# Kernel optimization log

Hardware: AMD Instinct MI355X
Metric: run time of the kernel (lower is better)

Reference implementation:

```python
import jax, jax.numpy as jnp
import numpy as np

EMBED = 1024

def setup_inputs() -> dict:
    key = jax.random.key(0)
    kx, kq, kk, kv = jax.random.split(key, 4)
    x = jax.random.normal(kx, (4, 2048, EMBED), dtype=jnp.float32)
    s = 1.0 / np.sqrt(EMBED)
    Wq = jax.random.normal(kq, (EMBED, EMBED), dtype=jnp.float32) * s
    Wk = jax.random.normal(kk, (EMBED, EMBED), dtype=jnp.float32) * s
    Wv = jax.random.normal(kv, (EMBED, EMBED), dtype=jnp.float32) * s
    return {"x": x, "Wq": Wq, "Wk": Wk, "Wv": Wv}

def reference(x, Wq, Wk, Wv):
    # x: [b, s, e]; nn.Linear(y) = y @ W.T, weights stored [out, in]
    Q = jnp.einsum('bse,oe->bso', x, Wq)
    K = jnp.einsum('bse,oe->bso', x, Wk)
    V = jnp.einsum('bse,oe->bso', x, Wv)
    scale = 1.0 / jnp.sqrt(jnp.asarray(x.shape[-1], x.dtype))
    energy = jnp.einsum('bqe,bke->bqk', Q, K) * scale  # [b, s, s]
    attention = jax.nn.softmax(energy, axis=-1)
    out = jnp.einsum('bqk,bke->bqe', attention, V)
    return out
```

## Files before the change

### kernel.cpp

```cpp
#include <hip/hip_runtime.h>
#include <stdint.h>


typedef __attribute__((ext_vector_type(8))) short bf16x8;
typedef __attribute__((ext_vector_type(4))) float f32x4;

__device__ __forceinline__ float bf2f(uint16_t u) {
    return __uint_as_float(((uint32_t)u) << 16);
}
__device__ __forceinline__ uint16_t f2bf(float f) {
    uint32_t u = __float_as_uint(f);
    uint32_t r = u + 0x7FFFu + ((u >> 16) & 1u);
    return (uint16_t)(r >> 16);
}

__device__ __forceinline__ void gll16(const void* g, void* l) {
    __builtin_amdgcn_global_load_lds(
        (const __attribute__((address_space(1))) uint32_t*)g,
        (__attribute__((address_space(3))) uint32_t*)l,
        16, 0, 0);
}

__global__ __launch_bounds__(256) void cast_f32_bf16(const float* __restrict__ in,
                                                     uint16_t* __restrict__ out,
                                                     int n4) {
    int i = blockIdx.x * 256 + threadIdx.x;
    if (i < n4) {
        float4 v = ((const float4*)in)[i];
        ushort4 o;
        o.x = f2bf(v.x); o.y = f2bf(v.y); o.z = f2bf(v.z); o.w = f2bf(v.w);
        ((ushort4*)out)[i] = o;
    }
}

__global__ __launch_bounds__(256) void transpose_bf16(const uint16_t* __restrict__ in,
                                                      uint16_t* __restrict__ out,
                                                      int rows, int cols) {
    __shared__ uint16_t tile[32][33];
    size_t bo = (size_t)blockIdx.z * rows * cols;
    in += bo; out += bo;
    int bx = blockIdx.x * 32;
    int by = blockIdx.y * 32;
    int tx = threadIdx.x, ty = threadIdx.y;
    #pragma unroll
    for (int i = ty; i < 32; i += 8)
        tile[i][tx] = in[(size_t)(by + i) * cols + bx + tx];
    __syncthreads();
    #pragma unroll
    for (int i = ty; i < 32; i += 8)
        out[(size_t)(bx + i) * rows + by + tx] = tile[tx][i];
}

__global__ __launch_bounds__(256) void softmax_rows(uint16_t* __restrict__ P) {
    const int n = 2048;
    uint16_t* row = P + (size_t)blockIdx.x * n;
    int tid = threadIdx.x;
    int w = tid >> 6, ln = tid & 63;
    float v[8];
    float m = -3.4e38f;
    #pragma unroll
    for (int i = 0; i < 8; i++) { v[i] = bf2f(row[tid + 256 * i]); m = fmaxf(m, v[i]); }
    #pragma unroll
    for (int o = 32; o >= 1; o >>= 1) m = fmaxf(m, __shfl_down(m, o, 64));
    __shared__ float smax[4], ssum[4];
    if (ln == 0) smax[w] = m;
    __syncthreads();
    m = fmaxf(fmaxf(smax[0], smax[1]), fmaxf(smax[2], smax[3]));
    float s = 0.f;
    #pragma unroll
    for (int i = 0; i < 8; i++) { v[i] = __expf(v[i] - m); s += v[i]; }
    #pragma unroll
    for (int o = 32; o >= 1; o >>= 1) s += __shfl_down(s, o, 64);
    if (ln == 0) ssum[w] = s;
    __syncthreads();
    s = ssum[0] + ssum[1] + ssum[2] + ssum[3];
    float inv = 1.f / s;
    #pragma unroll
    for (int i = 0; i < 8; i++) row[tid + 256 * i] = f2bf(v[i] * inv);
}

#define BM 128
#define BN 128
#define BK 32

template <typename OutT>
__global__ __launch_bounds__(256) void gemm_nt(const uint16_t* __restrict__ A,
                                               const uint16_t* __restrict__ B,
                                               OutT* __restrict__ C,
                                               int M, int N, int K, float alpha,
                                               long sA, long sB, long sC) {
    int bz = blockIdx.z;
    A += (long)bz * sA;
    B += (long)bz * sB;
    C += (long)bz * sC;

    __shared__ uint16_t As[2][BM * BK];
    __shared__ uint16_t Bs[2][BN * BK];

    const int tid  = threadIdx.x;
    const int m0   = blockIdx.y * BM;
    const int n0   = blockIdx.x * BN;
    const int wave = tid >> 6;
    const int lane = tid & 63;
    const int quad = lane >> 4;
    const int l16  = lane & 15;
    const int wr   = (wave >> 1) * 64;
    const int wc   = (wave & 1) * 64;

    const int sr = tid >> 2;
    const int sc = (tid & 3) * 8;
    const uint16_t* Ag = A + (long)(m0 + sr) * K + sc;
    const uint16_t* Bg = B + (long)(n0 + sr) * K + sc;
    const long rstep = (long)64 * K;
    const int so0 = sr * BK + sc;
    const int so1 = (sr + 64) * BK + sc;

    gll16(Ag,         &As[0][so0]);
    gll16(Ag + rstep, &As[0][so1]);
    gll16(Bg,         &Bs[0][so0]);
    gll16(Bg + rstep, &Bs[0][so1]);
    Ag += BK; Bg += BK;

    f32x4 acc[4][4] = {};
    const int nk = K / BK;

    for (int k = 0; k < nk; ++k) {
        const int cur = k & 1;
        __syncthreads();
        if (k + 1 < nk) {
            const int nxt = cur ^ 1;
            gll16(Ag,         &As[nxt][so0]);
            gll16(Ag + rstep, &As[nxt][so1]);
            gll16(Bg,         &Bs[nxt][so0]);
            gll16(Bg + rstep, &Bs[nxt][so1]);
            Ag += BK; Bg += BK;
        }

        const int ko = quad * 8;
        bf16x8 af[4], bfr[4];
        #pragma unroll
        for (int i = 0; i < 4; i++)
            af[i] = *(const bf16x8*)(&As[cur][(wr + i * 16 + l16) * BK + ko]);
        #pragma unroll
        for (int j = 0; j < 4; j++)
            bfr[j] = *(const bf16x8*)(&Bs[cur][(wc + j * 16 + l16) * BK + ko]);
        #pragma unroll
        for (int i = 0; i < 4; i++)
            #pragma unroll
            for (int j = 0; j < 4; j++)
                acc[i][j] = __builtin_amdgcn_mfma_f32_16x16x32_bf16(af[i], bfr[j], acc[i][j], 0, 0, 0);
    }

    #pragma unroll
    for (int i = 0; i < 4; i++) {
        #pragma unroll
        for (int j = 0; j < 4; j++) {
            #pragma unroll
            for (int r = 0; r < 4; r++) {
                int row = m0 + wr + i * 16 + quad * 4 + r;
                int col = n0 + wc + j * 16 + l16;
                float val = acc[i][j][r] * alpha;
                if constexpr (sizeof(OutT) == 2)
                    C[(long)row * N + col] = f2bf(val);
                else
                    C[(long)row * N + col] = val;
            }
        }
    }
}

extern "C" void kernel_launch(void* const* d_in, const int* in_sizes, int n_in,
                              void* d_out, int out_size, void* d_ws, size_t ws_size,
                              hipStream_t stream) {
    const float* x  = (const float*)d_in[0];
    const float* Wq = (const float*)d_in[1];
    const float* Wk = (const float*)d_in[2];
    const float* Wv = (const float*)d_in[3];
    float* out = (float*)d_out;

    const int Bn = 4, S = 2048, E = 1024;
    const long MS = (long)Bn * S;

    char* ws = (char*)d_ws;
    const size_t SZ_XB = (size_t)MS * E * 2;
    const size_t SZ_W  = (size_t)E * E * 2;
    const size_t SZ_P  = (size_t)Bn * S * S * 2;
    const size_t SZ_VT = (size_t)Bn * E * S * 2;
    uint16_t* xb  = (uint16_t*)ws;              ws += SZ_XB;
    uint16_t* wqb = (uint16_t*)ws;              ws += SZ_W;
    uint16_t* wkb = (uint16_t*)ws;              ws += SZ_W;
    uint16_t* wvb = (uint16_t*)ws;              ws += SZ_W;
    uint16_t* Qb  = (uint16_t*)ws;              ws += SZ_XB;
    uint16_t* Kb  = (uint16_t*)ws;              ws += SZ_XB;
    uint16_t* Vb  = (uint16_t*)ws;              ws += SZ_XB;
    uint16_t* Pb  = (uint16_t*)ws;              ws += SZ_P;
    uint16_t* Vt  = (uint16_t*)ws;              ws += SZ_VT;

    dim3 blk(256);

    {
        int n4 = (int)(MS * E / 4);
        cast_f32_bf16<<<dim3((n4 + 255) / 256), blk, 0, stream>>>(x, xb, n4);
        int n4w = E * E / 4;
        dim3 gw((n4w + 255) / 256);
        cast_f32_bf16<<<gw, blk, 0, stream>>>(Wq, wqb, n4w);
        cast_f32_bf16<<<gw, blk, 0, stream>>>(Wk, wkb, n4w);
        cast_f32_bf16<<<gw, blk, 0, stream>>>(Wv, wvb, n4w);
    }

    {
        dim3 g(E / BN, MS / BM, 1);
        gemm_nt<uint16_t><<<g, blk, 0, stream>>>(xb, wqb, Qb, (int)MS, E, E, 1.f, 0, 0, 0);
        gemm_nt<uint16_t><<<g, blk, 0, stream>>>(xb, wkb, Kb, (int)MS, E, E, 1.f, 0, 0, 0);
        gemm_nt<uint16_t><<<g, blk, 0, stream>>>(xb, wvb, Vb, (int)MS, E, E, 1.f, 0, 0, 0);
    }

    transpose_bf16<<<dim3(E / 32, S / 32, Bn), dim3(32, 8), 0, stream>>>(Vb, Vt, S, E);

    {
        dim3 g(S / BN, S / BM, Bn);
        gemm_nt<uint16_t><<<g, blk, 0, stream>>>(Qb, Kb, Pb, S, S, E, 0.03125f,
                                                 (long)S * E, (long)S * E, (long)S * S);
    }

    softmax_rows<<<dim3(Bn * S), blk, 0, stream>>>(Pb);

    {
        dim3 g(E / BN, S / BM, Bn);
        gemm_nt<float><<<g, blk, 0, stream>>>(Pb, Vt, out, S, E, S, 1.f,
                                              (long)S * S, (long)E * S, (long)S * E);
    }
}
```

Baseline: 312.1 us.

## Fuse QKV projections into one GEMM, triple-buffer loads, swizzle block order

The three Q/K/V projection GEMMs become a single GEMM against a concatenated [3E, E] weight, with strided leading dimensions so later kernels read Q, K and V directly from the fused buffer. The GEMM pipeline moves from double to triple buffering with explicit vmcnt waits and barriers, so two tiles are in flight at once. A 1D grid is remapped with an XCD-aware interleave and 8x8 supertile ordering to improve L2 locality. Together these cut launch count, raise occupancy of the projection launch, and hide more load latency, at the cost of more LDS per block and hand-written waitcnt assembly.

```diff
diff --git a/kernel.cpp b/kernel.cpp
--- a/kernel.cpp
+++ b/kernel.cpp
@@ -35,20 +35,21 @@
 
 __global__ __launch_bounds__(256) void transpose_bf16(const uint16_t* __restrict__ in,
                                                       uint16_t* __restrict__ out,
-                                                      int rows, int cols) {
+                                                      int rows, int cols, int istride,
+                                                      long ibatch, long obatch) {
     __shared__ uint16_t tile[32][33];
-    size_t bo = (size_t)blockIdx.z * rows * cols;
-    in += bo; out += bo;
+    in  += (long)blockIdx.z * ibatch;
+    out += (long)blockIdx.z * obatch;
     int bx = blockIdx.x * 32;
     int by = blockIdx.y * 32;
     int tx = threadIdx.x, ty = threadIdx.y;
     #pragma unroll
     for (int i = ty; i < 32; i += 8)
-        tile[i][tx] = in[(size_t)(by + i) * cols + bx + tx];
+        tile[i][tx] = in[(long)(by + i) * istride + bx + tx];
     __syncthreads();
     #pragma unroll
     for (int i = ty; i < 32; i += 8)
-        out[(size_t)(bx + i) * rows + by + tx] = tile[tx][i];
+        out[(long)(bx + i) * rows + by + tx] = tile[tx][i];
 }
 
 __global__ __launch_bounds__(256) void softmax_rows(uint16_t* __restrict__ P) {
@@ -87,19 +88,35 @@
 __global__ __launch_bounds__(256) void gemm_nt(const uint16_t* __restrict__ A,
                                                const uint16_t* __restrict__ B,
                                                OutT* __restrict__ C,
-                                               int M, int N, int K, float alpha,
+                                               int gx, int gy,
+                                               long lda, long ldb, long ldc,
+                                               int K, float alpha,
                                                long sA, long sB, long sC) {
-    int bz = blockIdx.z;
+    const int total = gridDim.x;
+    const int n     = blockIdx.x;
+    const int per   = total >> 3;
+    const int g     = (n & 7) * per + (n >> 3);
+    const int pb    = gx * gy;
+    const int bz    = g / pb;
+    const int r     = g - bz * pb;
+    const int stpr  = gx >> 3;
+    const int st    = r >> 6;
+    const int w     = r & 63;
+    const int sty   = st / stpr;
+    const int stx   = st - sty * stpr;
+    const int bx    = (stx << 3) + (w & 7);
+    const int by    = (sty << 3) + (w >> 3);
+
     A += (long)bz * sA;
     B += (long)bz * sB;
     C += (long)bz * sC;
 
-    __shared__ uint16_t As[2][BM * BK];
-    __shared__ uint16_t Bs[2][BN * BK];
+    __shared__ uint16_t As[3][BM * BK];
+    __shared__ uint16_t Bs[3][BM * BK];
 
     const int tid  = threadIdx.x;
-    const int m0   = blockIdx.y * BM;
-    const int n0   = blockIdx.x * BN;
+    const int m0   = by * BM;
+    const int n0   = bx * BN;
     const int wave = tid >> 6;
     const int lane = tid & 63;
     const int quad = lane >> 4;
@@ -109,46 +126,62 @@
 
     const int sr = tid >> 2;
     const int sc = (tid & 3) * 8;
-    const uint16_t* Ag = A + (long)(m0 + sr) * K + sc;
-    const uint16_t* Bg = B + (long)(n0 + sr) * K + sc;
-    const long rstep = (long)64 * K;
+    const uint16_t* Ag = A + (long)(m0 + sr) * lda + sc;
+    const uint16_t* Bg = B + (long)(n0 + sr) * ldb + sc;
+    const long rsA = 64 * lda;
+    const long rsB = 64 * ldb;
     const int so0 = sr * BK + sc;
     const int so1 = (sr + 64) * BK + sc;
 
-    gll16(Ag,         &As[0][so0]);
-    gll16(Ag + rstep, &As[0][so1]);
-    gll16(Bg,         &Bs[0][so0]);
-    gll16(Bg + rstep, &Bs[0][so1]);
+    const int nk = K / BK;
+
+    gll16(Ag,       &As[0][so0]);
+    gll16(Ag + rsA, &As[0][so1]);
+    gll16(Bg,       &Bs[0][so0]);
+    gll16(Bg + rsB, &Bs[0][so1]);
     Ag += BK; Bg += BK;
+    gll16(Ag,       &As[1][so0]);
+    gll16(Ag + rsA, &As[1][so1]);
+    gll16(Bg,       &Bs[1][so0]);
+    gll16(Bg + rsB, &Bs[1][so1]);
+    Ag += BK; Bg += BK;
 
     f32x4 acc[4][4] = {};
-    const int nk = K / BK;
+    int cur = 0, pf = 2;
 
     for (int k = 0; k < nk; ++k) {
-        const int cur = k & 1;
-        __syncthreads();
-        if (k + 1 < nk) {
-            const int nxt = cur ^ 1;
-            gll16(Ag,         &As[nxt][so0]);
-            gll16(Ag + rstep, &As[nxt][so1]);
-            gll16(Bg,         &Bs[nxt][so0]);
-            gll16(Bg + rstep, &Bs[nxt][so1]);
+        if (k < nk - 1) {
+            asm volatile("s_waitcnt vmcnt(4)\n\ts_barrier" ::: "memory");
+        } else {
+            asm volatile("s_waitcnt vmcnt(0)\n\ts_barrier" ::: "memory");
+        }
+
+        if (k + 2 < nk) {
+            gll16(Ag,       &As[pf][so0]);
+            gll16(Ag + rsA, &As[pf][so1]);
+            gll16(Bg,       &Bs[pf][so0]);
+            gll16(Bg + rsB, &Bs[pf][so1]);
             Ag += BK; Bg += BK;
         }
 
+        const uint16_t* Ac = As[cur];
+        const uint16_t* Bc = Bs[cur];
         const int ko = quad * 8;
         bf16x8 af[4], bfr[4];
         #pragma unroll
         for (int i = 0; i < 4; i++)
-            af[i] = *(const bf16x8*)(&As[cur][(wr + i * 16 + l16) * BK + ko]);
+            af[i] = *(const bf16x8*)(&Ac[(wr + i * 16 + l16) * BK + ko]);
         #pragma unroll
         for (int j = 0; j < 4; j++)
-            bfr[j] = *(const bf16x8*)(&Bs[cur][(wc + j * 16 + l16) * BK + ko]);
+            bfr[j] = *(const bf16x8*)(&Bc[(wc + j * 16 + l16) * BK + ko]);
         #pragma unroll
         for (int i = 0; i < 4; i++)
             #pragma unroll
             for (int j = 0; j < 4; j++)
                 acc[i][j] = __builtin_amdgcn_mfma_f32_16x16x32_bf16(af[i], bfr[j], acc[i][j], 0, 0, 0);
+
+        cur = (cur == 2) ? 0 : cur + 1;
+        pf  = (pf  == 2) ? 0 : pf + 1;
     }
 
     #pragma unroll
@@ -156,14 +189,14 @@
         #pragma unroll
         for (int j = 0; j < 4; j++) {
             #pragma unroll
-            for (int r = 0; r < 4; r++) {
-                int row = m0 + wr + i * 16 + quad * 4 + r;
+            for (int r4 = 0; r4 < 4; r4++) {
+                int row = m0 + wr + i * 16 + quad * 4 + r4;
                 int col = n0 + wc + j * 16 + l16;
-                float val = acc[i][j][r] * alpha;
+                float val = acc[i][j][r4] * alpha;
                 if constexpr (sizeof(OutT) == 2)
-                    C[(long)row * N + col] = f2bf(val);
+                    C[(long)row * ldc + col] = f2bf(val);
                 else
-                    C[(long)row * N + col] = val;
+                    C[(long)row * ldc + col] = val;
             }
         }
     }
@@ -180,21 +213,14 @@
 
     const int Bn = 4, S = 2048, E = 1024;
     const long MS = (long)Bn * S;
+    const int  N3 = 3 * E;
 
     char* ws = (char*)d_ws;
-    const size_t SZ_XB = (size_t)MS * E * 2;
-    const size_t SZ_W  = (size_t)E * E * 2;
-    const size_t SZ_P  = (size_t)Bn * S * S * 2;
-    const size_t SZ_VT = (size_t)Bn * E * S * 2;
-    uint16_t* xb  = (uint16_t*)ws;              ws += SZ_XB;
-    uint16_t* wqb = (uint16_t*)ws;              ws += SZ_W;
-    uint16_t* wkb = (uint16_t*)ws;              ws += SZ_W;
-    uint16_t* wvb = (uint16_t*)ws;              ws += SZ_W;
-    uint16_t* Qb  = (uint16_t*)ws;              ws += SZ_XB;
-    uint16_t* Kb  = (uint16_t*)ws;              ws += SZ_XB;
-    uint16_t* Vb  = (uint16_t*)ws;              ws += SZ_XB;
-    uint16_t* Pb  = (uint16_t*)ws;              ws += SZ_P;
-    uint16_t* Vt  = (uint16_t*)ws;              ws += SZ_VT;
+    uint16_t* xb    = (uint16_t*)ws;  ws += (size_t)MS * E * 2;
+    uint16_t* wqkvb = (uint16_t*)ws;  ws += (size_t)N3 * E * 2;
+    uint16_t* QKVb  = (uint16_t*)ws;  ws += (size_t)MS * N3 * 2;
+    uint16_t* Pb    = (uint16_t*)ws;  ws += (size_t)Bn * S * S * 2;
+    uint16_t* Vt    = (uint16_t*)ws;  ws += (size_t)Bn * E * S * 2;
 
     dim3 blk(256);
 
@@ -203,31 +229,33 @@
         cast_f32_bf16<<<dim3((n4 + 255) / 256), blk, 0, stream>>>(x, xb, n4);
         int n4w = E * E / 4;
         dim3 gw((n4w + 255) / 256);
-        cast_f32_bf16<<<gw, blk, 0, stream>>>(Wq, wqb, n4w);
-        cast_f32_bf16<<<gw, blk, 0, stream>>>(Wk, wkb, n4w);
-        cast_f32_bf16<<<gw, blk, 0, stream>>>(Wv, wvb, n4w);
-    }
-
-    {
-        dim3 g(E / BN, MS / BM, 1);
-        gemm_nt<uint16_t><<<g, blk, 0, stream>>>(xb, wqb, Qb, (int)MS, E, E, 1.f, 0, 0, 0);
-        gemm_nt<uint16_t><<<g, blk, 0, stream>>>(xb, wkb, Kb, (int)MS, E, E, 1.f, 0, 0, 0);
-        gemm_nt<uint16_t><<<g, blk, 0, stream>>>(xb, wvb, Vb, (int)MS, E, E, 1.f, 0, 0, 0);
-    }
-
-    transpose_bf16<<<dim3(E / 32, S / 32, Bn), dim3(32, 8), 0, stream>>>(Vb, Vt, S, E);
-
-    {
-        dim3 g(S / BN, S / BM, Bn);
-        gemm_nt<uint16_t><<<g, blk, 0, stream>>>(Qb, Kb, Pb, S, S, E, 0.03125f,
-                                                 (long)S * E, (long)S * E, (long)S * S);
+        cast_f32_bf16<<<gw, blk, 0, stream>>>(Wq, wqkvb,             n4w);
+        cast_f32_bf16<<<gw, blk, 0, stream>>>(Wk, wqkvb + (size_t)E * E,     n4w);
+        cast_f32_bf16<<<gw, blk, 0, stream>>>(Wv, wqkvb + (size_t)2 * E * E, n4w);
+    }
+
+    {
+        int gx = N3 / BN, gy = (int)(MS / BM);
+        gemm_nt<uint16_t><<<dim3(gx * gy), blk, 0, stream>>>(
+            xb, wqkvb, QKVb, gx, gy, E, E, N3, E, 1.f, 0, 0, 0);
+    }
+
+    transpose_bf16<<<dim3(E / 32, S / 32, Bn), dim3(32, 8), 0, stream>>>(
+        QKVb + 2 * E, Vt, S, E, N3, (long)S * N3, (long)E * S);
+
+    {
+        int gx = S / BN, gy = S / BM;
+        gemm_nt<uint16_t><<<dim3(gx * gy * Bn), blk, 0, stream>>>(
+            QKVb, QKVb + E, Pb, gx, gy, N3, N3, S, E, 0.03125f,
+            (long)S * N3, (long)S * N3, (long)S * S);
     }
 
     softmax_rows<<<dim3(Bn * S), blk, 0, stream>>>(Pb);
 
     {
-        dim3 g(E / BN, S / BM, Bn);
-        gemm_nt<float><<<g, blk, 0, stream>>>(Pb, Vt, out, S, E, S, 1.f,
-                                              (long)S * S, (long)E * S, (long)S * E);
-    }
-}
+        int gx = E / BN, gy = S / BM;
+        gemm_nt<float><<<dim3(gx * gy * Bn), blk, 0, stream>>>(
+            Pb, Vt, out, gx, gy, S, S, E, S, 1.f,
+            (long)S * S, (long)E * S, (long)S * E);
+    }
+}
```

New measurement: 278.6 us. -10.7%, faster.
